# Optimization experiments

Hardware: AMD Instinct MI355X
Metric: run time of the kernel (lower is better)

## Reference

```python
import jax, jax.numpy as jnp
import numpy as np

B, T, I, U, O = 128, 2048, 128, 256, 128
KILL = (3, 7)  # kill_neuron list: zero these hidden units after each step


def setup_inputs() -> dict:
    key = jax.random.key(0)
    ks = jax.random.split(key, 7)
    s = 1.0 / np.sqrt(U)  # torch nn.RNN / nn.Linear default uniform init bound
    u = lambda k, sh: jax.random.uniform(k, sh, jnp.float32, -s, s)
    return {
        "x": jax.random.normal(ks[0], (B, T, I), jnp.float32),
        "W_ih": u(ks[1], (U, I)),
        "W_hh": u(ks[2], (U, U)),
        "b_ih": u(ks[3], (U,)),
        "b_hh": u(ks[4], (U,)),
        "W_fc": u(ks[5], (O, U)),
        "b_fc": u(ks[6], (O,)),
    }


def reference(x, W_ih, W_hh, b_ih, b_hh, W_fc, b_fc):
    units = W_hh.shape[0]
    mask = jnp.ones((units,), x.dtype).at[jnp.array(KILL)].set(0.0)
    h0 = jnp.zeros((x.shape[0], units), x.dtype)  # initial_state=None -> zeros
    # Precompute input projection for all timesteps: [B,T,U] -> scan xs [T,B,U]
    x_proj = jnp.einsum('bti,ui->btu', x, W_ih) + b_ih + b_hh

    def step(h, xt):  # xt: [B,U]
        h_raw = jnp.tanh(xt + h @ W_hh.T)   # rnn output 'temp' (unmasked)
        h_masked = h_raw * mask             # kill_neuron applied to carried hidden
        return h_masked, (h_raw, h_masked)

    _, (h_raw_seq, h_masked_seq) = jax.lax.scan(step, h0, jnp.swapaxes(x_proj, 0, 1))
    # readout is fc(temp) i.e. applied to the UNMASKED per-step output
    readouts = jnp.einsum('tbu,ou->bto', h_raw_seq, W_fc) + b_fc  # [B,T,O]
    hs = jnp.swapaxes(h_masked_seq, 0, 1)  # [B,T,U] (masked hidden states)
    return readouts, hs
```

## Files before the change

kernel.cpp:

```cpp
#include <hip/hip_runtime.h>
#include <math.h>

#define BB 128
#define TT 2048
#define II 128
#define UU 256
#define OO 128

typedef __attribute__((ext_vector_type(8))) short bf16x8;
typedef __attribute__((ext_vector_type(4))) float f32x4;

#define MFMA16(a, b, cacc) __builtin_amdgcn_mfma_f32_16x16x32_bf16(a, b, cacc, 0, 0, 0)

__device__ __forceinline__ void bar_lds() {
    __builtin_amdgcn_sched_barrier(0);
    asm volatile("s_waitcnt lgkmcnt(0)" ::: "memory");
    __builtin_amdgcn_s_barrier();
    __builtin_amdgcn_sched_barrier(0);
}

__device__ __forceinline__ short f2bf(float f) {
    unsigned u = __float_as_uint(f);
    unsigned r = (u + 0x7FFFu + ((u >> 16) & 1u)) >> 16;
    return (short)r;
}

__device__ __forceinline__ bf16x8 loadf8(const float* p) {
    float4 va = *reinterpret_cast<const float4*>(p);
    float4 vb = *reinterpret_cast<const float4*>(p + 4);
    bf16x8 v;
    v[0] = f2bf(va.x); v[1] = f2bf(va.y); v[2] = f2bf(va.z); v[3] = f2bf(va.w);
    v[4] = f2bf(vb.x); v[5] = f2bf(vb.y); v[6] = f2bf(vb.z); v[7] = f2bf(vb.w);
    return v;
}

__global__ __launch_bounds__(256, 2) void k_inproj(
    const float* __restrict__ x, const float* __restrict__ Wih,
    const float* __restrict__ bih, const float* __restrict__ bhh,
    float* __restrict__ xp)
{
    __shared__ __align__(16) short xs[64 * 128];
    const int tid = threadIdx.x;
    const int w = tid >> 6;
    const int lane = tid & 63;
    const int g = lane >> 4;
    const int c = lane & 15;
    bf16x8 wb[4][4];
    float bias[4];
    #pragma unroll
    for (int nt = 0; nt < 4; ++nt) {
        const int u = w * 64 + nt * 16 + c;
        #pragma unroll
        for (int kt = 0; kt < 4; ++kt)
            wb[nt][kt] = loadf8(&Wih[(size_t)u * II + kt * 32 + g * 8]);
        bias[nt] = bih[u] + bhh[u];
    }
    const int srow = tid >> 2, sq = tid & 3;
    const int ntiles = (BB * TT) / 64;
    for (int tile = blockIdx.x; tile < ntiles; tile += gridDim.x) {
        const size_t rowbase = (size_t)tile * 64;
        #pragma unroll
        for (int t2 = 0; t2 < 4; ++t2) {
            int n = sq * 4 + t2;
            const float* src = &x[(rowbase + srow) * II + n * 8];
            bf16x8 v = loadf8(src);
            int off = srow * 128 + ((n * 8) ^ ((srow & 7) << 3));
            *reinterpret_cast<bf16x8*>(&xs[off]) = v;
        }
        __syncthreads();
        #pragma unroll
        for (int mt = 0; mt < 4; ++mt) {
            const int row = mt * 16 + c;
            bf16x8 af[4];
            #pragma unroll
            for (int kt = 0; kt < 4; ++kt)
                af[kt] = *reinterpret_cast<const bf16x8*>(
                    &xs[row * 128 + ((kt * 32 + g * 8) ^ ((c & 7) << 3))]);
            f32x4 acc[4];
            #pragma unroll
            for (int nt = 0; nt < 4; ++nt) acc[nt] = (f32x4){0.f,0.f,0.f,0.f};
            #pragma unroll
            for (int kt = 0; kt < 4; ++kt)
                #pragma unroll
                for (int nt = 0; nt < 4; ++nt)
                    acc[nt] = MFMA16(af[kt], wb[nt][kt], acc[nt]);
            #pragma unroll
            for (int nt = 0; nt < 4; ++nt)
                #pragma unroll
                for (int r = 0; r < 4; ++r)
                    xp[(rowbase + mt * 16 + g * 4 + r) * UU + w * 64 + nt * 16 + c]
                        = acc[nt][r] + bias[nt];
        }
        __syncthreads();
    }
}

__global__ __launch_bounds__(512, 2) void k_rnn(
    const float* __restrict__ Whh, float* __restrict__ xph)
{
    __shared__ __align__(16) short hbuf[2 * 256];
    const int tid = threadIdx.x;
    const int w = tid >> 6;
    const int lane = tid & 63;
    const int g = lane >> 4;
    const int c = lane & 15;
    bf16x8 bq[2][8];
    #pragma unroll
    for (int q2 = 0; q2 < 2; ++q2) {
        const int ub = w * 32 + q2 * 16 + c;
        #pragma unroll
        for (int kt = 0; kt < 8; ++kt)
            bq[q2][kt] = loadf8(&Whh[(size_t)ub * UU + kt * 32 + g * 8]);
    }
    const int q = g & 1;
    const int uxp = w * 32 + q * 16 + c;
    const bool gl = (g < 2);
    const bool kill = (uxp == 3) || (uxp == 7);

    if (tid < 256) reinterpret_cast<int*>(hbuf)[tid] = 0;
    __syncthreads();

    float* rowp = xph + (size_t)blockIdx.x * (size_t)TT * UU;
    float xpv = rowp[uxp];
    float xpn = rowp[UU + uxp];

    auto step = [&](int t, int p) {
        int tn = t + 2; tn = (tn < TT) ? tn : (TT - 1);
        float xpn2 = rowp[(size_t)tn * UU + uxp];
        const bf16x8* hb = reinterpret_cast<const bf16x8*>(hbuf + p * 256);
        f32x4 acc0[4], acc1[4];
        #pragma unroll
        for (int i = 0; i < 4; ++i) {
            acc0[i] = (f32x4){0.f, 0.f, 0.f, 0.f};
            acc1[i] = (f32x4){0.f, 0.f, 0.f, 0.f};
        }
        #pragma unroll
        for (int kt = 0; kt < 8; ++kt) {
            bf16x8 a = hb[kt * 4 + g];
            acc0[kt & 3] = MFMA16(a, bq[0][kt], acc0[kt & 3]);
            acc1[kt & 3] = MFMA16(a, bq[1][kt], acc1[kt & 3]);
        }
        float d0 = (acc0[0][0] + acc0[1][0]) + (acc0[2][0] + acc0[3][0]);
        float d1 = (acc1[0][0] + acc1[1][0]) + (acc1[2][0] + acc1[3][0]);
        float Dres = q ? d1 : d0;
        float s = Dres + xpv;
        float hr = 1.0f - 2.0f / (__expf(2.0f * s) + 1.0f);
        if (gl) {
            rowp[(size_t)t * UU + uxp] = hr;
        } else {
            hbuf[(p ^ 1) * 256 + uxp] = kill ? (short)0 : f2bf(hr);
        }
        bar_lds();
        xpv = xpn; xpn = xpn2;
    };
    for (int t = 0; t < TT; t += 2) { step(t, 0); step(t + 1, 1); }
}

__global__ __launch_bounds__(256, 2) void k_readout(
    const float* __restrict__ Wfc, const float* __restrict__ bfc,
    float* __restrict__ hraw, float* __restrict__ outR)
{
    __shared__ __align__(16) short hs[64 * 256];
    const int tid = threadIdx.x;
    const int w = tid >> 6;
    const int lane = tid & 63;
    const int g = lane >> 4;
    const int c = lane & 15;
    bf16x8 wb[2][8];
    float bias[2];
    #pragma unroll
    for (int nt = 0; nt < 2; ++nt) {
        const int o = w * 32 + nt * 16 + c;
        #pragma unroll
        for (int kt = 0; kt < 8; ++kt)
            wb[nt][kt] = loadf8(&Wfc[(size_t)o * UU + kt * 32 + g * 8]);
        bias[nt] = bfc[o];
    }
    const int srow = tid >> 2, sq = tid & 3;
    const int ntiles = (BB * TT) / 64;
    for (int tile = blockIdx.x; tile < ntiles; tile += gridDim.x) {
        const size_t rowbase = (size_t)tile * 64;
        #pragma unroll
        for (int t2 = 0; t2 < 8; ++t2) {
            int n = sq * 8 + t2;
            const float* src = &hraw[(rowbase + srow) * UU + n * 8];
            bf16x8 v = loadf8(src);
            int off = srow * 256 + ((n * 8) ^ ((srow & 7) << 3));
            *reinterpret_cast<bf16x8*>(&hs[off]) = v;
        }
        __syncthreads();
        if (tid < 128) {
            int r = tid >> 1, col = (tid & 1) ? 7 : 3;
            hraw[(rowbase + r) * UU + col] = 0.f;
        }
        #pragma unroll
        for (int mt = 0; mt < 4; ++mt) {
            const int row = mt * 16 + c;
            f32x4 acc[2];
            acc[0] = (f32x4){0.f,0.f,0.f,0.f};
            acc[1] = (f32x4){0.f,0.f,0.f,0.f};
            #pragma unroll
            for (int kt = 0; kt < 8; ++kt) {
                bf16x8 af = *reinterpret_cast<const bf16x8*>(
                    &hs[row * 256 + ((kt * 32 + g * 8) ^ ((c & 7) << 3))]);
                acc[0] = MFMA16(af, wb[0][kt], acc[0]);
                acc[1] = MFMA16(af, wb[1][kt], acc[1]);
            }
            #pragma unroll
            for (int nt = 0; nt < 2; ++nt)
                #pragma unroll
                for (int r = 0; r < 4; ++r)
                    outR[(rowbase + mt * 16 + g * 4 + r) * OO + w * 32 + nt * 16 + c]
                        = acc[nt][r] + bias[nt];
        }
        __syncthreads();
    }
}

extern "C" void kernel_launch(void* const* d_in, const int* in_sizes, int n_in,
                              void* d_out, int out_size, void* d_ws, size_t ws_size,
                              hipStream_t stream) {
    const float* x   = (const float*)d_in[0];
    const float* Wih = (const float*)d_in[1];
    const float* Whh = (const float*)d_in[2];
    const float* bih = (const float*)d_in[3];
    const float* bhh = (const float*)d_in[4];
    const float* Wfc = (const float*)d_in[5];
    const float* bfc = (const float*)d_in[6];
    float* outR = (float*)d_out;
    float* outH = outR + (size_t)BB * TT * OO;

    k_inproj<<<512, 256, 0, stream>>>(x, Wih, bih, bhh, outH);
    k_rnn<<<128, 512, 0, stream>>>(Whh, outH);
    k_readout<<<512, 256, 0, stream>>>(Wfc, bfc, outH, outR);
}
```

Measured before the change: 1.254 ms.

## Halve RNN block to four waves, each computing 64 hidden units per step

The recurrent kernel now runs with 256 threads (4 wavefronts) per batch row instead of 512. Each wave holds 64 columns of W_hh in registers and computes 4 output tiles per step, with each lane producing two hidden units. The goal is cheaper per-step barriers with fewer waves and more MFMA work per wave. The cost is higher register pressure and more serial MFMA work per wave on the critical path.

Result: slower. 1.320 ms (+5.3%).

```diff
diff --git a/kernel.cpp b/kernel.cpp
--- a/kernel.cpp
+++ b/kernel.cpp
@@ -95,7 +95,7 @@
     }
 }
 
-__global__ __launch_bounds__(512, 2) void k_rnn(
+__global__ __launch_bounds__(256, 1) void k_rnn(
     const float* __restrict__ Whh, float* __restrict__ xph)
 {
     __shared__ __align__(16) short hbuf[2 * 256];
@@ -104,54 +104,67 @@
     const int lane = tid & 63;
     const int g = lane >> 4;
     const int c = lane & 15;
-    bf16x8 bq[2][8];
+    bf16x8 bq[4][8];
     #pragma unroll
-    for (int q2 = 0; q2 < 2; ++q2) {
-        const int ub = w * 32 + q2 * 16 + c;
+    for (int nt = 0; nt < 4; ++nt) {
+        const int ub = w * 64 + nt * 16 + c;
         #pragma unroll
         for (int kt = 0; kt < 8; ++kt)
-            bq[q2][kt] = loadf8(&Whh[(size_t)ub * UU + kt * 32 + g * 8]);
-    }
-    const int q = g & 1;
-    const int uxp = w * 32 + q * 16 + c;
+            bq[nt][kt] = loadf8(&Whh[(size_t)ub * UU + kt * 32 + g * 8]);
+    }
+    const int uA = w * 64 + (g & 1) * 32 + c;
+    const int uB = uA + 16;
     const bool gl = (g < 2);
-    const bool kill = (uxp == 3) || (uxp == 7);
-
+    const bool killA = (uA == 3) || (uA == 7);
     if (tid < 256) reinterpret_cast<int*>(hbuf)[tid] = 0;
     __syncthreads();
 
     float* rowp = xph + (size_t)blockIdx.x * (size_t)TT * UU;
-    float xpv = rowp[uxp];
-    float xpn = rowp[UU + uxp];
+    float xpvA = rowp[uA],      xpvB = rowp[uB];
+    float xpnA = rowp[UU + uA], xpnB = rowp[UU + uB];
 
     auto step = [&](int t, int p) {
         int tn = t + 2; tn = (tn < TT) ? tn : (TT - 1);
-        float xpn2 = rowp[(size_t)tn * UU + uxp];
+        float xpn2A = rowp[(size_t)tn * UU + uA];
+        float xpn2B = rowp[(size_t)tn * UU + uB];
         const bf16x8* hb = reinterpret_cast<const bf16x8*>(hbuf + p * 256);
-        f32x4 acc0[4], acc1[4];
-        #pragma unroll
-        for (int i = 0; i < 4; ++i) {
-            acc0[i] = (f32x4){0.f, 0.f, 0.f, 0.f};
-            acc1[i] = (f32x4){0.f, 0.f, 0.f, 0.f};
-        }
-        #pragma unroll
-        for (int kt = 0; kt < 8; ++kt) {
-            bf16x8 a = hb[kt * 4 + g];
-            acc0[kt & 3] = MFMA16(a, bq[0][kt], acc0[kt & 3]);
-            acc1[kt & 3] = MFMA16(a, bq[1][kt], acc1[kt & 3]);
-        }
-        float d0 = (acc0[0][0] + acc0[1][0]) + (acc0[2][0] + acc0[3][0]);
-        float d1 = (acc1[0][0] + acc1[1][0]) + (acc1[2][0] + acc1[3][0]);
-        float Dres = q ? d1 : d0;
-        float s = Dres + xpv;
-        float hr = 1.0f - 2.0f / (__expf(2.0f * s) + 1.0f);
+        f32x4 a0a = {0.f,0.f,0.f,0.f}, a0b = {0.f,0.f,0.f,0.f};
+        f32x4 a1a = {0.f,0.f,0.f,0.f}, a1b = {0.f,0.f,0.f,0.f};
+        f32x4 a2a = {0.f,0.f,0.f,0.f}, a2b = {0.f,0.f,0.f,0.f};
+        f32x4 a3a = {0.f,0.f,0.f,0.f}, a3b = {0.f,0.f,0.f,0.f};
+        #pragma unroll
+        for (int kt = 0; kt < 8; kt += 2) {
+            bf16x8 f0 = hb[kt * 4 + g];
+            bf16x8 f1 = hb[(kt + 1) * 4 + g];
+            a0a = MFMA16(f0, bq[0][kt],     a0a);
+            a1a = MFMA16(f0, bq[1][kt],     a1a);
+            a2a = MFMA16(f0, bq[2][kt],     a2a);
+            a3a = MFMA16(f0, bq[3][kt],     a3a);
+            a0b = MFMA16(f1, bq[0][kt + 1], a0b);
+            a1b = MFMA16(f1, bq[1][kt + 1], a1b);
+            a2b = MFMA16(f1, bq[2][kt + 1], a2b);
+            a3b = MFMA16(f1, bq[3][kt + 1], a3b);
+        }
+        float d0 = a0a[0] + a0b[0];
+        float d1 = a1a[0] + a1b[0];
+        float d2 = a2a[0] + a2b[0];
+        float d3 = a3a[0] + a3b[0];
+        float dA = (g & 1) ? d2 : d0;
+        float dB = (g & 1) ? d3 : d1;
+        float sA = dA + xpvA;
+        float sB = dB + xpvB;
+        float hrA = 1.0f - 2.0f / (__expf(2.0f * sA) + 1.0f);
+        float hrB = 1.0f - 2.0f / (__expf(2.0f * sB) + 1.0f);
         if (gl) {
-            rowp[(size_t)t * UU + uxp] = hr;
+            rowp[(size_t)t * UU + uA] = hrA;
+            rowp[(size_t)t * UU + uB] = hrB;
         } else {
-            hbuf[(p ^ 1) * 256 + uxp] = kill ? (short)0 : f2bf(hr);
+            hbuf[(p ^ 1) * 256 + uA] = killA ? (short)0 : f2bf(hrA);
+            hbuf[(p ^ 1) * 256 + uB] = f2bf(hrB);
         }
         bar_lds();
-        xpv = xpn; xpn = xpn2;
+        xpvA = xpnA; xpnA = xpn2A;
+        xpvB = xpnB; xpnB = xpn2B;
     };
     for (int t = 0; t < TT; t += 2) { step(t, 0); step(t + 1, 1); }
 }
@@ -231,6 +244,6 @@
     float* outH = outR + (size_t)BB * TT * OO;
 
     k_inproj<<<512, 256, 0, stream>>>(x, Wih, bih, bhh, outH);
-    k_rnn<<<128, 512, 0, stream>>>(Whh, outH);
+    k_rnn<<<128, 256, 0, stream>>>(Whh, outH);
     k_readout<<<512, 256, 0, stream>>>(Wfc, bfc, outH, outR);
 }
```

## Fuse input projection, recurrence and readout into one persistent flag-synchronized kernel

Applied to the files above, without the earlier changes.

Replaces three sequential kernels with a single launch of 256 blocks. 128 blocks run the recurrence, one per batch row, while 128 helper blocks compute that row's input projection in 64-step chunks ahead of it and then run the readout behind it. The two sides coordinate through acquire/release progress flags in workspace memory. This hides the projection and readout work under the serial recurrence and removes launch gaps, but it relies on all 256 blocks being co-resident (otherwise spin-waits could deadlock) and adds spin polling plus a memset.

Result: slower. 2.426 ms (+93.4%).

```diff
diff --git a/kernel.cpp b/kernel.cpp
--- a/kernel.cpp
+++ b/kernel.cpp
@@ -34,186 +34,199 @@
     return v;
 }
 
-__global__ __launch_bounds__(256, 2) void k_inproj(
+__global__ __launch_bounds__(512, 2) void k_all(
     const float* __restrict__ x, const float* __restrict__ Wih,
-    const float* __restrict__ bih, const float* __restrict__ bhh,
-    float* __restrict__ xp)
+    const float* __restrict__ Whh, const float* __restrict__ bih,
+    const float* __restrict__ bhh, const float* __restrict__ Wfc,
+    const float* __restrict__ bfc, float* __restrict__ outR,
+    float* __restrict__ outH, int* __restrict__ flags)
 {
-    __shared__ __align__(16) short xs[64 * 128];
+    __shared__ __align__(16) short lds16[64 * 256];
     const int tid = threadIdx.x;
     const int w = tid >> 6;
     const int lane = tid & 63;
     const int g = lane >> 4;
     const int c = lane & 15;
-    bf16x8 wb[4][4];
-    float bias[4];
-    #pragma unroll
-    for (int nt = 0; nt < 4; ++nt) {
-        const int u = w * 64 + nt * 16 + c;
+    int* prog   = flags;
+    int* xpdone = flags + 128;
+
+    if (blockIdx.x < 128) {
+        const int b = blockIdx.x;
+        short* hbuf = lds16;
+        bf16x8 bq[2][8];
         #pragma unroll
-        for (int kt = 0; kt < 4; ++kt)
-            wb[nt][kt] = loadf8(&Wih[(size_t)u * II + kt * 32 + g * 8]);
-        bias[nt] = bih[u] + bhh[u];
-    }
-    const int srow = tid >> 2, sq = tid & 3;
-    const int ntiles = (BB * TT) / 64;
-    for (int tile = blockIdx.x; tile < ntiles; tile += gridDim.x) {
-        const size_t rowbase = (size_t)tile * 64;
-        #pragma unroll
-        for (int t2 = 0; t2 < 4; ++t2) {
-            int n = sq * 4 + t2;
-            const float* src = &x[(rowbase + srow) * II + n * 8];
-            bf16x8 v = loadf8(src);
-            int off = srow * 128 + ((n * 8) ^ ((srow & 7) << 3));
-            *reinterpret_cast<bf16x8*>(&xs[off]) = v;
+        for (int q2 = 0; q2 < 2; ++q2) {
+            const int ub = w * 32 + q2 * 16 + c;
+            #pragma unroll
+            for (int kt = 0; kt < 8; ++kt)
+                bq[q2][kt] = loadf8(&Whh[(size_t)ub * UU + kt * 32 + g * 8]);
         }
+        const int q = g & 1;
+        const int uxp = w * 32 + q * 16 + c;
+        const bool gl = (g < 2);
+        const bool kill = (uxp == 3) || (uxp == 7);
+        if (tid < 256) reinterpret_cast<int*>(hbuf)[tid] = 0;
         __syncthreads();
-        #pragma unroll
-        for (int mt = 0; mt < 4; ++mt) {
-            const int row = mt * 16 + c;
-            bf16x8 af[4];
-            #pragma unroll
-            for (int kt = 0; kt < 4; ++kt)
-                af[kt] = *reinterpret_cast<const bf16x8*>(
-                    &xs[row * 128 + ((kt * 32 + g * 8) ^ ((c & 7) << 3))]);
-            f32x4 acc[4];
-            #pragma unroll
-            for (int nt = 0; nt < 4; ++nt) acc[nt] = (f32x4){0.f,0.f,0.f,0.f};
-            #pragma unroll
-            for (int kt = 0; kt < 4; ++kt)
-                #pragma unroll
-                for (int nt = 0; nt < 4; ++nt)
-                    acc[nt] = MFMA16(af[kt], wb[nt][kt], acc[nt]);
-            #pragma unroll
-            for (int nt = 0; nt < 4; ++nt)
-                #pragma unroll
-                for (int r = 0; r < 4; ++r)
-                    xp[(rowbase + mt * 16 + g * 4 + r) * UU + w * 64 + nt * 16 + c]
-                        = acc[nt][r] + bias[nt];
+
+        float* rowp = outH + (size_t)b * (size_t)TT * UU;
+        while (__hip_atomic_load(&xpdone[b], __ATOMIC_ACQUIRE,
+                                 __HIP_MEMORY_SCOPE_AGENT) < 1)
+            __builtin_amdgcn_s_sleep(8);
+        float xpv = rowp[uxp];
+        float xpn = rowp[UU + uxp];
+
+        auto step = [&](int t, int p) {
+            int tn = t + 2; tn = (tn < TT) ? tn : (TT - 1);
+            if ((tn & 63) == 0) {
+                const int need = (tn >> 6) + 1;
+                while (__hip_atomic_load(&xpdone[b], __ATOMIC_ACQUIRE,
+                                         __HIP_MEMORY_SCOPE_AGENT) < need)
+                    __builtin_amdgcn_s_sleep(2);
+            }
+            float xpn2 = rowp[(size_t)tn * UU + uxp];
+            const bf16x8* hb = reinterpret_cast<const bf16x8*>(hbuf + p * 256);
+            f32x4 acc0[4], acc1[4];
+            #pragma unroll
+            for (int i = 0; i < 4; ++i) {
+                acc0[i] = (f32x4){0.f, 0.f, 0.f, 0.f};
+                acc1[i] = (f32x4){0.f, 0.f, 0.f, 0.f};
+            }
+            #pragma unroll
+            for (int kt = 0; kt < 8; ++kt) {
+                bf16x8 a = hb[kt * 4 + g];
+                acc0[kt & 3] = MFMA16(a, bq[0][kt], acc0[kt & 3]);
+                acc1[kt & 3] = MFMA16(a, bq[1][kt], acc1[kt & 3]);
+            }
+            float d0 = (acc0[0][0] + acc0[1][0]) + (acc0[2][0] + acc0[3][0]);
+            float d1 = (acc1[0][0] + acc1[1][0]) + (acc1[2][0] + acc1[3][0]);
+            float Dres = q ? d1 : d0;
+            float s = Dres + xpv;
+            float hr = 1.0f - 2.0f / (__expf(2.0f * s) + 1.0f);
+            if (gl) {
+                rowp[(size_t)t * UU + uxp] = hr;
+            } else {
+                hbuf[(p ^ 1) * 256 + uxp] = kill ? (short)0 : f2bf(hr);
+            }
+            const bool flag = ((t & 63) == 63);
+            if (flag) asm volatile("s_waitcnt vmcnt(0)" ::: "memory");
+            bar_lds();
+            if (flag && tid == 0)
+                __hip_atomic_store(&prog[b], (t >> 6) + 1, __ATOMIC_RELEASE,
+                                   __HIP_MEMORY_SCOPE_AGENT);
+            xpv = xpn; xpn = xpn2;
+        };
+        for (int t = 0; t < TT; t += 2) { step(t, 0); step(t + 1, 1); }
+    } else {
+        const int b = blockIdx.x - 128;
+        const int nrole = w & 3;
+        const int mh = w >> 2;
+        const int srow = tid >> 3, sq = tid & 7;
+        {
+            bf16x8 wb[4][4];
+            float bias[4];
+            #pragma unroll
+            for (int nt = 0; nt < 4; ++nt) {
+                const int u = nrole * 64 + nt * 16 + c;
+                #pragma unroll
+                for (int kt = 0; kt < 4; ++kt)
+                    wb[nt][kt] = loadf8(&Wih[(size_t)u * II + kt * 32 + g * 8]);
+                bias[nt] = bih[u] + bhh[u];
+            }
+            for (int s = 0; s < 32; ++s) {
+                const size_t rowbase = (size_t)b * TT + (size_t)s * 64;
+                #pragma unroll
+                for (int t2 = 0; t2 < 2; ++t2) {
+                    int n = sq * 2 + t2;
+                    bf16x8 v = loadf8(&x[(rowbase + srow) * II + n * 8]);
+                    int off = srow * 128 + ((n * 8) ^ ((srow & 7) << 3));
+                    *reinterpret_cast<bf16x8*>(&lds16[off]) = v;
+                }
+                __syncthreads();
+                #pragma unroll
+                for (int mi = 0; mi < 2; ++mi) {
+                    const int mt = mh * 2 + mi;
+                    const int row = mt * 16 + c;
+                    bf16x8 af[4];
+                    #pragma unroll
+                    for (int kt = 0; kt < 4; ++kt)
+                        af[kt] = *reinterpret_cast<const bf16x8*>(
+                            &lds16[row * 128 + ((kt * 32 + g * 8) ^ ((c & 7) << 3))]);
+                    f32x4 acc[4];
+                    #pragma unroll
+                    for (int nt = 0; nt < 4; ++nt) acc[nt] = (f32x4){0.f,0.f,0.f,0.f};
+                    #pragma unroll
+                    for (int kt = 0; kt < 4; ++kt)
+                        #pragma unroll
+                        for (int nt = 0; nt < 4; ++nt)
+                            acc[nt] = MFMA16(af[kt], wb[nt][kt], acc[nt]);
+                    #pragma unroll
+                    for (int nt = 0; nt < 4; ++nt)
+                        #pragma unroll
+                        for (int r = 0; r < 4; ++r)
+                            outH[(rowbase + mt * 16 + g * 4 + r) * UU
+                                 + nrole * 64 + nt * 16 + c] = acc[nt][r] + bias[nt];
+                }
+                asm volatile("s_waitcnt vmcnt(0)" ::: "memory");
+                __syncthreads();
+                if (tid == 0)
+                    __hip_atomic_store(&xpdone[b], s + 1, __ATOMIC_RELEASE,
+                                       __HIP_MEMORY_SCOPE_AGENT);
+                __syncthreads();
+            }
         }
-        __syncthreads();
-    }
-}
-
-__global__ __launch_bounds__(512, 2) void k_rnn(
-    const float* __restrict__ Whh, float* __restrict__ xph)
-{
-    __shared__ __align__(16) short hbuf[2 * 256];
-    const int tid = threadIdx.x;
-    const int w = tid >> 6;
-    const int lane = tid & 63;
-    const int g = lane >> 4;
-    const int c = lane & 15;
-    bf16x8 bq[2][8];
-    #pragma unroll
-    for (int q2 = 0; q2 < 2; ++q2) {
-        const int ub = w * 32 + q2 * 16 + c;
-        #pragma unroll
-        for (int kt = 0; kt < 8; ++kt)
-            bq[q2][kt] = loadf8(&Whh[(size_t)ub * UU + kt * 32 + g * 8]);
-    }
-    const int q = g & 1;
-    const int uxp = w * 32 + q * 16 + c;
-    const bool gl = (g < 2);
-    const bool kill = (uxp == 3) || (uxp == 7);
-
-    if (tid < 256) reinterpret_cast<int*>(hbuf)[tid] = 0;
-    __syncthreads();
-
-    float* rowp = xph + (size_t)blockIdx.x * (size_t)TT * UU;
-    float xpv = rowp[uxp];
-    float xpn = rowp[UU + uxp];
-
-    auto step = [&](int t, int p) {
-        int tn = t + 2; tn = (tn < TT) ? tn : (TT - 1);
-        float xpn2 = rowp[(size_t)tn * UU + uxp];
-        const bf16x8* hb = reinterpret_cast<const bf16x8*>(hbuf + p * 256);
-        f32x4 acc0[4], acc1[4];
-        #pragma unroll
-        for (int i = 0; i < 4; ++i) {
-            acc0[i] = (f32x4){0.f, 0.f, 0.f, 0.f};
-            acc1[i] = (f32x4){0.f, 0.f, 0.f, 0.f};
+        {
+            bf16x8 wb[2][8];
+            float bias[2];
+            #pragma unroll
+            for (int nt = 0; nt < 2; ++nt) {
+                const int o = nrole * 32 + nt * 16 + c;
+                #pragma unroll
+                for (int kt = 0; kt < 8; ++kt)
+                    wb[nt][kt] = loadf8(&Wfc[(size_t)o * UU + kt * 32 + g * 8]);
+                bias[nt] = bfc[o];
+            }
+            float* hraw = outH;
+            for (int s = 0; s < 32; ++s) {
+                while (__hip_atomic_load(&prog[b], __ATOMIC_ACQUIRE,
+                                         __HIP_MEMORY_SCOPE_AGENT) < s + 1)
+                    __builtin_amdgcn_s_sleep(8);
+                const size_t rowbase = (size_t)b * TT + (size_t)s * 64;
+                #pragma unroll
+                for (int t2 = 0; t2 < 4; ++t2) {
+                    int n = sq * 4 + t2;
+                    bf16x8 v = loadf8(&hraw[(rowbase + srow) * UU + n * 8]);
+                    int off = srow * 256 + ((n * 8) ^ ((srow & 7) << 3));
+                    *reinterpret_cast<bf16x8*>(&lds16[off]) = v;
+                }
+                __syncthreads();
+                if (tid < 128) {
+                    int r = tid >> 1, col = (tid & 1) ? 7 : 3;
+                    hraw[(rowbase + r) * UU + col] = 0.f;
+                }
+                #pragma unroll
+                for (int mi = 0; mi < 2; ++mi) {
+                    const int mt = mh * 2 + mi;
+                    const int row = mt * 16 + c;
+                    f32x4 acc[2];
+                    acc[0] = (f32x4){0.f,0.f,0.f,0.f};
+                    acc[1] = (f32x4){0.f,0.f,0.f,0.f};
+                    #pragma unroll
+                    for (int kt = 0; kt < 8; ++kt) {
+                        bf16x8 af = *reinterpret_cast<const bf16x8*>(
+                            &lds16[row * 256 + ((kt * 32 + g * 8) ^ ((c & 7) << 3))]);
+                        acc[0] = MFMA16(af, wb[0][kt], acc[0]);
+                        acc[1] = MFMA16(af, wb[1][kt], acc[1]);
+                    }
+                    #pragma unroll
+                    for (int nt = 0; nt < 2; ++nt)
+                        #pragma unroll
+                        for (int r = 0; r < 4; ++r)
+                            outR[(rowbase + mt * 16 + g * 4 + r) * OO
+                                 + nrole * 32 + nt * 16 + c] = acc[nt][r] + bias[nt];
+                }
+                __syncthreads();
+            }
         }
-        #pragma unroll
-        for (int kt = 0; kt < 8; ++kt) {
-            bf16x8 a = hb[kt * 4 + g];
-            acc0[kt & 3] = MFMA16(a, bq[0][kt], acc0[kt & 3]);
-            acc1[kt & 3] = MFMA16(a, bq[1][kt], acc1[kt & 3]);
-        }
-        float d0 = (acc0[0][0] + acc0[1][0]) + (acc0[2][0] + acc0[3][0]);
-        float d1 = (acc1[0][0] + acc1[1][0]) + (acc1[2][0] + acc1[3][0]);
-        float Dres = q ? d1 : d0;
-        float s = Dres + xpv;
-        float hr = 1.0f - 2.0f / (__expf(2.0f * s) + 1.0f);
-        if (gl) {
-            rowp[(size_t)t * UU + uxp] = hr;
-        } else {
-            hbuf[(p ^ 1) * 256 + uxp] = kill ? (short)0 : f2bf(hr);
-        }
-        bar_lds();
-        xpv = xpn; xpn = xpn2;
-    };
-    for (int t = 0; t < TT; t += 2) { step(t, 0); step(t + 1, 1); }
-}
-
-__global__ __launch_bounds__(256, 2) void k_readout(
-    const float* __restrict__ Wfc, const float* __restrict__ bfc,
-    float* __restrict__ hraw, float* __restrict__ outR)
-{
-    __shared__ __align__(16) short hs[64 * 256];
-    const int tid = threadIdx.x;
-    const int w = tid >> 6;
-    const int lane = tid & 63;
-    const int g = lane >> 4;
-    const int c = lane & 15;
-    bf16x8 wb[2][8];
-    float bias[2];
-    #pragma unroll
-    for (int nt = 0; nt < 2; ++nt) {
-        const int o = w * 32 + nt * 16 + c;
-        #pragma unroll
-        for (int kt = 0; kt < 8; ++kt)
-            wb[nt][kt] = loadf8(&Wfc[(size_t)o * UU + kt * 32 + g * 8]);
-        bias[nt] = bfc[o];
-    }
-    const int srow = tid >> 2, sq = tid & 3;
-    const int ntiles = (BB * TT) / 64;
-    for (int tile = blockIdx.x; tile < ntiles; tile += gridDim.x) {
-        const size_t rowbase = (size_t)tile * 64;
-        #pragma unroll
-        for (int t2 = 0; t2 < 8; ++t2) {
-            int n = sq * 8 + t2;
-            const float* src = &hraw[(rowbase + srow) * UU + n * 8];
-            bf16x8 v = loadf8(src);
-            int off = srow * 256 + ((n * 8) ^ ((srow & 7) << 3));
-            *reinterpret_cast<bf16x8*>(&hs[off]) = v;
-        }
-        __syncthreads();
-        if (tid < 128) {
-            int r = tid >> 1, col = (tid & 1) ? 7 : 3;
-            hraw[(rowbase + r) * UU + col] = 0.f;
-        }
-        #pragma unroll
-        for (int mt = 0; mt < 4; ++mt) {
-            const int row = mt * 16 + c;
-            f32x4 acc[2];
-            acc[0] = (f32x4){0.f,0.f,0.f,0.f};
-            acc[1] = (f32x4){0.f,0.f,0.f,0.f};
-            #pragma unroll
-            for (int kt = 0; kt < 8; ++kt) {
-                bf16x8 af = *reinterpret_cast<const bf16x8*>(
-                    &hs[row * 256 + ((kt * 32 + g * 8) ^ ((c & 7) << 3))]);
-                acc[0] = MFMA16(af, wb[0][kt], acc[0]);
-                acc[1] = MFMA16(af, wb[1][kt], acc[1]);
-            }
-            #pragma unroll
-            for (int nt = 0; nt < 2; ++nt)
-                #pragma unroll
-                for (int r = 0; r < 4; ++r)
-                    outR[(rowbase + mt * 16 + g * 4 + r) * OO + w * 32 + nt * 16 + c]
-                        = acc[nt][r] + bias[nt];
-        }
-        __syncthreads();
     }
 }
 
@@ -229,8 +242,9 @@
     const float* bfc = (const float*)d_in[6];
     float* outR = (float*)d_out;
     float* outH = outR + (size_t)BB * TT * OO;
-
-    k_inproj<<<512, 256, 0, stream>>>(x, Wih, bih, bhh, outH);
-    k_rnn<<<128, 512, 0, stream>>>(Whh, outH);
-    k_readout<<<512, 256, 0, stream>>>(Wfc, bfc, outH, outR);
-}
+    int* flags = (int*)d_ws;
+
+    hipMemsetAsync(d_ws, 0, 1024, stream);
+    k_all<<<256, 512, 0, stream>>>(x, Wih, Whh, bih, bhh, Wfc, bfc,
+                                   outR, outH, flags);
+}
```

## Process two batch rows per RNN block to interleave independent recurrences

Applied to the files above, without the earlier changes.

The recurrent kernel now handles two batch sequences per workgroup (rows b and b+64), launching 64 blocks instead of 128. Each step issues MFMAs for both sequences against the shared register-resident W_hh, so two independent dependency chains interleave and hide MFMA, tanh and barrier latency. The cost is half as many blocks, leaving CUs idle on a 256-CU part, plus more registers and per-step work for each block.

Result: slower. 1.781 ms (+42.0%).

```diff
diff --git a/kernel.cpp b/kernel.cpp
--- a/kernel.cpp
+++ b/kernel.cpp
@@ -95,10 +95,10 @@
     }
 }
 
-__global__ __launch_bounds__(512, 2) void k_rnn(
+__global__ __launch_bounds__(512, 2) void k_rnn2(
     const float* __restrict__ Whh, float* __restrict__ xph)
 {
-    __shared__ __align__(16) short hbuf[2 * 256];
+    __shared__ __align__(16) short hbuf[2][2 * 256];
     const int tid = threadIdx.x;
     const int w = tid >> 6;
     const int lane = tid & 63;
@@ -117,41 +117,58 @@
     const bool gl = (g < 2);
     const bool kill = (uxp == 3) || (uxp == 7);
 
-    if (tid < 256) reinterpret_cast<int*>(hbuf)[tid] = 0;
+    if (tid < 256) {
+        reinterpret_cast<int*>(hbuf[0])[tid] = 0;
+        reinterpret_cast<int*>(hbuf[1])[tid] = 0;
+    }
     __syncthreads();
 
-    float* rowp = xph + (size_t)blockIdx.x * (size_t)TT * UU;
-    float xpv = rowp[uxp];
-    float xpn = rowp[UU + uxp];
+    float* rowpA = xph + (size_t)blockIdx.x * (size_t)TT * UU;
+    float* rowpB = xph + (size_t)(blockIdx.x + 64) * (size_t)TT * UU;
+    float xpvA = rowpA[uxp],      xpvB = rowpB[uxp];
+    float xpnA = rowpA[UU + uxp], xpnB = rowpB[UU + uxp];
 
     auto step = [&](int t, int p) {
         int tn = t + 2; tn = (tn < TT) ? tn : (TT - 1);
-        float xpn2 = rowp[(size_t)tn * UU + uxp];
-        const bf16x8* hb = reinterpret_cast<const bf16x8*>(hbuf + p * 256);
-        f32x4 acc0[4], acc1[4];
+        float xpn2A = rowpA[(size_t)tn * UU + uxp];
+        float xpn2B = rowpB[(size_t)tn * UU + uxp];
+        const bf16x8* hbA = reinterpret_cast<const bf16x8*>(hbuf[0] + p * 256);
+        const bf16x8* hbB = reinterpret_cast<const bf16x8*>(hbuf[1] + p * 256);
+        f32x4 accA0[4], accA1[4], accB0[4], accB1[4];
         #pragma unroll
         for (int i = 0; i < 4; ++i) {
-            acc0[i] = (f32x4){0.f, 0.f, 0.f, 0.f};
-            acc1[i] = (f32x4){0.f, 0.f, 0.f, 0.f};
+            accA0[i] = (f32x4){0.f, 0.f, 0.f, 0.f};
+            accA1[i] = (f32x4){0.f, 0.f, 0.f, 0.f};
+            accB0[i] = (f32x4){0.f, 0.f, 0.f, 0.f};
+            accB1[i] = (f32x4){0.f, 0.f, 0.f, 0.f};
         }
         #pragma unroll
         for (int kt = 0; kt < 8; ++kt) {
-            bf16x8 a = hb[kt * 4 + g];
-            acc0[kt & 3] = MFMA16(a, bq[0][kt], acc0[kt & 3]);
-            acc1[kt & 3] = MFMA16(a, bq[1][kt], acc1[kt & 3]);
-        }
-        float d0 = (acc0[0][0] + acc0[1][0]) + (acc0[2][0] + acc0[3][0]);
-        float d1 = (acc1[0][0] + acc1[1][0]) + (acc1[2][0] + acc1[3][0]);
-        float Dres = q ? d1 : d0;
-        float s = Dres + xpv;
-        float hr = 1.0f - 2.0f / (__expf(2.0f * s) + 1.0f);
+            bf16x8 aA = hbA[kt * 4 + g];
+            bf16x8 aB = hbB[kt * 4 + g];
+            accA0[kt & 3] = MFMA16(aA, bq[0][kt], accA0[kt & 3]);
+            accA1[kt & 3] = MFMA16(aA, bq[1][kt], accA1[kt & 3]);
+            accB0[kt & 3] = MFMA16(aB, bq[0][kt], accB0[kt & 3]);
+            accB1[kt & 3] = MFMA16(aB, bq[1][kt], accB1[kt & 3]);
+        }
+        float dA0 = (accA0[0][0] + accA0[1][0]) + (accA0[2][0] + accA0[3][0]);
+        float dA1 = (accA1[0][0] + accA1[1][0]) + (accA1[2][0] + accA1[3][0]);
+        float dB0 = (accB0[0][0] + accB0[1][0]) + (accB0[2][0] + accB0[3][0]);
+        float dB1 = (accB1[0][0] + accB1[1][0]) + (accB1[2][0] + accB1[3][0]);
+        float sA = (q ? dA1 : dA0) + xpvA;
+        float sB = (q ? dB1 : dB0) + xpvB;
+        float hrA = 1.0f - 2.0f / (__expf(2.0f * sA) + 1.0f);
+        float hrB = 1.0f - 2.0f / (__expf(2.0f * sB) + 1.0f);
         if (gl) {
-            rowp[(size_t)t * UU + uxp] = hr;
+            rowpA[(size_t)t * UU + uxp] = hrA;
+            rowpB[(size_t)t * UU + uxp] = hrB;
         } else {
-            hbuf[(p ^ 1) * 256 + uxp] = kill ? (short)0 : f2bf(hr);
+            hbuf[0][(p ^ 1) * 256 + uxp] = kill ? (short)0 : f2bf(hrA);
+            hbuf[1][(p ^ 1) * 256 + uxp] = kill ? (short)0 : f2bf(hrB);
         }
         bar_lds();
-        xpv = xpn; xpn = xpn2;
+        xpvA = xpnA; xpnA = xpn2A;
+        xpvB = xpnB; xpnB = xpn2B;
     };
     for (int t = 0; t < TT; t += 2) { step(t, 0); step(t + 1, 1); }
 }
@@ -231,6 +248,6 @@
     float* outH = outR + (size_t)BB * TT * OO;
 
     k_inproj<<<512, 256, 0, stream>>>(x, Wih, bih, bhh, outH);
-    k_rnn<<<128, 512, 0, stream>>>(Whh, outH);
+    k_rnn2<<<64, 512, 0, stream>>>(Whh, outH);
     k_readout<<<512, 256, 0, stream>>>(Wfc, bfc, outH, outR);
 }
```
